# Kernel optimization log

Measured on AMD Instinct MI355X. Metric: run time of the kernel, lower is better.

## Reference

```python
import jax, jax.numpy as jnp
import numpy as np

N_NODES = 50000
SEQ_LEN = 20
INPUT_DIM = 16
HIDDEN = 128
LATENT = 64
N_EDGES = 800000


def setup_inputs() -> dict:
    key = jax.random.key(0)
    ks = iter(jax.random.split(key, 64))
    def p(shape, scale=0.05):
        return jax.random.normal(next(ks), shape, dtype=jnp.float32) * scale
    inp = {}
    inp['track_sequences'] = jax.random.normal(next(ks), (N_NODES, SEQ_LEN, INPUT_DIM), dtype=jnp.float32)
    inp['edge_index'] = jax.random.randint(next(ks), (2, N_EDGES), 0, N_NODES, dtype=jnp.int64)
    # LSTM (2 layers, torch gate order i,f,g,o)
    inp['lstm_Wih0'] = p((4 * HIDDEN, INPUT_DIM)); inp['lstm_Whh0'] = p((4 * HIDDEN, HIDDEN))
    inp['lstm_bih0'] = p((4 * HIDDEN,));            inp['lstm_bhh0'] = p((4 * HIDDEN,))
    inp['lstm_Wih1'] = p((4 * HIDDEN, HIDDEN));     inp['lstm_Whh1'] = p((4 * HIDDEN, HIDDEN))
    inp['lstm_bih1'] = p((4 * HIDDEN,));            inp['lstm_bhh1'] = p((4 * HIDDEN,))
    # encoder MLP: hidden->hidden->latent
    inp['enc_W1'] = p((HIDDEN, HIDDEN)); inp['enc_b1'] = p((HIDDEN,))
    inp['enc_W2'] = p((HIDDEN, LATENT)); inp['enc_b2'] = p((LATENT,))
    # 3 GCN layers
    inp['gcn_W0'] = p((LATENT, HIDDEN)); inp['gcn_b0'] = p((HIDDEN,))
    inp['gcn_W1'] = p((HIDDEN, HIDDEN)); inp['gcn_b1'] = p((HIDDEN,))
    inp['gcn_W2'] = p((HIDDEN, HIDDEN)); inp['gcn_b2'] = p((HIDDEN,))
    # edge predictor MLP: 2H -> H -> H/2 -> 1 (sigmoid)
    inp['e_W1'] = p((2 * HIDDEN, HIDDEN)); inp['e_b1'] = p((HIDDEN,))
    inp['e_W2'] = p((HIDDEN, HIDDEN // 2)); inp['e_b2'] = p((HIDDEN // 2,))
    inp['e_W3'] = p((HIDDEN // 2, 1)); inp['e_b3'] = p((1,))
    # classifier: H -> H/2 -> 4
    inp['c_W1'] = p((HIDDEN, HIDDEN // 2)); inp['c_b1'] = p((HIDDEN // 2,))
    inp['c_W2'] = p((HIDDEN // 2, 4)); inp['c_b2'] = p((4,))
    # uncertainty: H -> H/2 -> 1 (softplus)
    inp['u_W1'] = p((HIDDEN, HIDDEN // 2)); inp['u_b1'] = p((HIDDEN // 2,))
    inp['u_W2'] = p((HIDDEN // 2, 1)); inp['u_b2'] = p((1,))
    return inp


def _lstm_layer(x, Wih, Whh, bih, bhh):
    # x: [N, T, Din]; torch gate order i, f, g, o
    n, t, _ = x.shape
    h_dim = Whh.shape[1]
    xg = jnp.einsum('ntd,gd->ntg', x, Wih) + bih  # [N, T, 4H] precomputed input part
    def step(carry, xt):
        h, c = carry
        g = xt + h @ Whh.T + bhh
        i, f, gg, o = jnp.split(g, 4, axis=-1)
        c = jax.nn.sigmoid(f) * c + jax.nn.sigmoid(i) * jnp.tanh(gg)
        h = jax.nn.sigmoid(o) * jnp.tanh(c)
        return (h, c), h
    h0 = jnp.zeros((n, h_dim), x.dtype)
    (_, _), hs = jax.lax.scan(step, (h0, h0), jnp.swapaxes(xg, 0, 1))
    return jnp.swapaxes(hs, 0, 1)  # [N, T, H]


def _gcn(x, W, b, src, dst, num_nodes):
    # PyG GCNConv: self-loops, symmetric deg^-1/2 normalization
    x = x @ W  # [N, out]
    loop = jnp.arange(num_nodes, dtype=src.dtype)
    s = jnp.concatenate([src, loop])
    d = jnp.concatenate([dst, loop])
    deg = jax.ops.segment_sum(jnp.ones_like(d, x.dtype), d, num_segments=num_nodes)
    dinv = jax.lax.rsqrt(jnp.maximum(deg, 1.0))  # deg >= 1 due to self-loops
    norm = dinv[s] * dinv[d]  # [E+N]
    out = jax.ops.segment_sum(x[s] * norm[:, None], d, num_segments=num_nodes)
    return out + b


def reference(track_sequences, edge_index,
              lstm_Wih0, lstm_Whh0, lstm_bih0, lstm_bhh0,
              lstm_Wih1, lstm_Whh1, lstm_bih1, lstm_bhh1,
              enc_W1, enc_b1, enc_W2, enc_b2,
              gcn_W0, gcn_b0, gcn_W1, gcn_b1, gcn_W2, gcn_b2,
              e_W1, e_b1, e_W2, e_b2, e_W3, e_b3,
              c_W1, c_b1, c_W2, c_b2,
              u_W1, u_b1, u_W2, u_b2):
    n = track_sequences.shape[0]
    # --- TrackEncoder (eval mode: LSTM inter-layer dropout inactive) ---
    h = _lstm_layer(track_sequences, lstm_Wih0, lstm_Whh0, lstm_bih0, lstm_bhh0)
    h = _lstm_layer(h, lstm_Wih1, lstm_Whh1, lstm_bih1, lstm_bhh1)
    final_hidden = h[:, -1]  # [N, H]
    latent = jax.nn.relu(final_hidden @ enc_W1 + enc_b1) @ enc_W2 + enc_b2  # [N, L]
    # --- GCN stack (eval mode: dropout inactive) ---
    src, dst = edge_index[0], edge_index[1]
    x = latent
    for W, b in ((gcn_W0, gcn_b0), (gcn_W1, gcn_b1), (gcn_W2, gcn_b2)):
        x = jax.nn.relu(_gcn(x, W, b, src, dst, n))
    # --- edge predictor ---
    ef = jnp.concatenate([x[src], x[dst]], axis=1)  # [E, 2H]
    ef = jax.nn.relu(ef @ e_W1 + e_b1)
    ef = jax.nn.relu(ef @ e_W2 + e_b2)
    edge_pred = jax.nn.sigmoid(ef @ e_W3 + e_b3)  # [E, 1]
    # --- classifier & uncertainty heads ---
    track_classes = jax.nn.relu(x @ c_W1 + c_b1) @ c_W2 + c_b2  # [N, 4]
    uncertainties = jax.nn.softplus(jax.nn.relu(x @ u_W1 + u_b1) @ u_W2 + u_b2)  # [N, 1]
    return (x, edge_pred, track_classes, uncertainties)
```

## Files before the change

kernel.cpp:

```cpp
#include <hip/hip_runtime.h>
#include <math.h>

typedef float f32x4 __attribute__((ext_vector_type(4)));
typedef short s16x8 __attribute__((ext_vector_type(8)));
typedef unsigned short u16;

__device__ __forceinline__ float sigmoid_(float x) { return 1.f / (1.f + __expf(-x)); }
__device__ __forceinline__ float tanh_(float x) {
  float e = __expf(-2.f * x);
  return fmaf(2.f, 1.f / (1.f + e), -1.f);
}
__device__ __forceinline__ float softplus_(float x) {
  return (x > 15.f) ? x : log1pf(__expf(x));
}
__device__ __forceinline__ u16 f2bf(float f) {
  unsigned u = __float_as_uint(f);
  u += 0x7fffu + ((u >> 16) & 1u);
  return (u16)(u >> 16);
}
__device__ __forceinline__ float bf2f(u16 u) {
  return __uint_as_float((unsigned)u << 16);
}
#define PIN4(x) asm volatile("" : "+v"(x))

__global__ void prep_lstm_w(const float* __restrict__ Wih0, const float* __restrict__ Whh0,
                            const float* __restrict__ Wih1, const float* __restrict__ Whh1,
                            const float* __restrict__ bih0, const float* __restrict__ bhh0,
                            const float* __restrict__ bih1, const float* __restrict__ bhh1,
                            u16* __restrict__ Wp0, u16* __restrict__ Wp1,
                            float* __restrict__ bs0, float* __restrict__ bs1)
{
  int idx = blockIdx.x * 256 + threadIdx.x;
  if (idx < 20 * 512 * 8) {
    int c = idx >> 12, rem = idx & 4095;
    int col = rem >> 3, e = rem & 7;
    int k = c * 8 + e;
    float v = 0.f;
    if (k < 16) v = Wih0[col * 16 + k];
    else if (k >= 32) v = Whh0[col * 128 + (k - 32)];
    Wp0[idx] = f2bf(v);
  }
  int i1 = idx - 20 * 512 * 8;
  if (i1 >= 0 && i1 < 32 * 512 * 8) {
    int c = i1 >> 12, rem = i1 & 4095;
    int col = rem >> 3, e = rem & 7;
    int k = c * 8 + e;
    float v = (k < 128) ? Wih1[col * 128 + k] : Whh1[col * 128 + (k - 128)];
    Wp1[i1] = f2bf(v);
  }
  int i2 = idx - 52 * 512 * 8;
  if (i2 >= 0 && i2 < 512) bs0[i2] = bih0[i2] + bhh0[i2];
  int i3 = i2 - 512;
  if (i3 >= 0 && i3 < 512) bs1[i3] = bih1[i3] + bhh1[i3];
}

__global__ void pack_w(const float* __restrict__ W, u16* __restrict__ Wp, int K, int C) {
// ... 27 lines not shown
    cuW2p[j] = f2bf(v);
  }
  int j2 = idx - (128 * 128 + 2048);
  if (j2 >= 0 && j2 < 128) cub1[j2] = (j2 < 64) ? cb1[j2] : ub1[j2 - 64];
  int j3 = j2 - 128;
  if (j3 >= 0 && j3 < 16) cub2[j3] = (j3 < 4) ? cb2[j3] : (j3 == 4 ? ub2[0] : 0.f);
}

__device__ __forceinline__ void epi2(const f32x4 (&acc)[2][4], f32x4* cs,
    const float (&bs)[4], u16* ldsw, int uoff, int kq, int mh,
    int nodebase, float* hf, int u, int n, bool last)
{
#pragma unroll
  for (int mm = 0; mm < 2; ++mm) {
#pragma unroll
    for (int r = 0; r < 4; ++r) {
      float gi = acc[mm][0][r] + bs[0];
      float gf = acc[mm][1][r] + bs[1];
      float gg = acc[mm][2][r] + bs[2];
      float go = acc[mm][3][r] + bs[3];
      float c = sigmoid_(gf) * cs[mm][r] + sigmoid_(gi) * tanh_(gg);
      cs[mm][r] = c;
      float h = sigmoid_(go) * tanh_(c);
      int node = (mh * 2 + mm) * 16 + kq * 4 + r;
      ldsw[uoff + node * 8] = f2bf(h);
      if (last) {
        int gn = nodebase + node;
        if (gn < n) hf[(size_t)gn * 128 + u] = h;
      }
    }
  }
}

__global__ __launch_bounds__(512, 2) void lstm_l0(
    const float* __restrict__ seq, const u16* __restrict__ Wp0,
    const float* __restrict__ bs0, u16* __restrict__ h0seq,
    int n, int tile0, int ntiles)
{
  __shared__ __align__(16) u16 A0[2 * 20 * 512];
  const int RSZ = 20 * 512;
  const int tid = threadIdx.x;
  const int l = tid & 63;
  const int wq = __builtin_amdgcn_readfirstlane(tid >> 6);
  const int kq = l >> 4;
  const int la = (l & 15) * 8;
  const int colu = wq * 16 + (l & 15);
  const int uoff = (4 + (colu >> 3)) * 512 + (colu & 7);

  s16x8 b0[5][4];
#pragma unroll
  for (int kc = 0; kc < 5; ++kc)
#pragma unroll
    for (int g = 0; g < 4; ++g) {
      b0[kc][g] = *(const s16x8*)&Wp0[(size_t)(kc * 4 + kq) * 4096 + (g * 128 + colu) * 8];
      PIN4(b0[kc][g]);
    }
  float bsr[4];
#pragma unroll
  for (int g = 0; g < 4; ++g) bsr[g] = bs0[g * 128 + colu];
  const f32x4 zero4 = {0.f, 0.f, 0.f, 0.f};

  for (int tt = blockIdx.x; tt < ntiles; tt += gridDim.x) {
    const int nodebase = (tile0 + tt) * 64;
    const int nld = min(nodebase + (tid >> 2), n - 1);
    u16* __restrict__ hdst = h0seq + (size_t)tt * 20 * 8192;
    for (int i = tid; i < 18 * 512; i += 512) A0[2 * 512 + i] = 0;
    for (int i = tid; i < 2 * 512; i += 512) A0[RSZ + 2 * 512 + i] = 0;
    if (tid < 256) {
      int nd = tid >> 2, q = tid & 3;
      f32x4 v = __builtin_nontemporal_load((const f32x4*)(seq + (size_t)nld * 320 + q * 4));
      unsigned d0 = (unsigned)f2bf(v[0]) | ((unsigned)f2bf(v[1]) << 16);
      unsigned d1 = (unsigned)f2bf(v[2]) | ((unsigned)f2bf(v[3]) << 16);
      unsigned* dstp = (unsigned*)&A0[(q >> 1) * 512 + nd * 8 + (q & 1) * 4];
      dstp[0] = d0; dstp[1] = d1;
    }
    f32x4 c0[4];
#pragma unroll
    for (int m = 0; m < 4; ++m) c0[m] = zero4;
    __syncthreads();

    for (int t = 0; t < 20; ++t) {
      const int base_r = (t & 1) * RSZ;
      const int base_w = ((t + 1) & 1) * RSZ;
      f32x4 xnext;
      const bool ldx = (t < 19) && (tid < 256);
      if (ldx) xnext = __builtin_nontemporal_load(
          (const f32x4*)(seq + (size_t)nld * 320 + (t + 1) * 16 + (tid & 3) * 4));
      if (t >= 1) {
        s16x8 u0 = *(const s16x8*)&A0[base_r + 2048 + tid * 8];
        s16x8 u1 = *(const s16x8*)&A0[base_r + 2048 + 4096 + tid * 8];
        __builtin_nontemporal_store(u0, (s16x8*)&hdst[(size_t)(t - 1) * 8192 + tid * 8]);
        __builtin_nontemporal_store(u1, (s16x8*)&hdst[(size_t)(t - 1) * 8192 + 4096 + tid * 8]);
      }
#pragma unroll
      for (int mh = 0; mh < 2; ++mh) {
        f32x4 acc[2][4];
#pragma unroll
        for (int mm = 0; mm < 2; ++mm)
#pragma unroll
          for (int g = 0; g < 4; ++g) acc[mm][g] = zero4;
#pragma unroll
        for (int kc = 0; kc < 5; ++kc) {
          const int ch = kc * 4 + kq;
          s16x8 av[2];
#pragma unroll
          for (int mm = 0; mm < 2; ++mm)
            av[mm] = *(const s16x8*)&A0[base_r + ch * 512 + (mh * 2 + mm) * 128 + la];
#pragma unroll
          for (int g = 0; g < 4; ++g)
#pragma unroll
            for (int mm = 0; mm < 2; ++mm)
              acc[mm][g] = __builtin_amdgcn_mfma_f32_16x16x32_bf16(av[mm], b0[kc][g], acc[mm][g], 0, 0, 0);
        }
        epi2(acc, &c0[mh * 2], bsr, &A0[base_w], uoff, kq, mh, 0, nullptr, colu, 0, false);
      }
      if (ldx) {
        int nd = tid >> 2, q = tid & 3;
        unsigned d0 = (unsigned)f2bf(xnext[0]) | ((unsigned)f2bf(xnext[1]) << 16);
        unsigned d1 = (unsigned)f2bf(xnext[2]) | ((unsigned)f2bf(xnext[3]) << 16);
        unsigned* dstp = (unsigned*)&A0[base_w + (q >> 1) * 512 + nd * 8 + (q & 1) * 4];
        dstp[0] = d0; dstp[1] = d1;
      }
      __syncthreads();
    }
    {
      s16x8 u0 = *(const s16x8*)&A0[2048 + tid * 8];
      s16x8 u1 = *(const s16x8*)&A0[2048 + 4096 + tid * 8];
      __builtin_nontemporal_store(u0, (s16x8*)&hdst[(size_t)19 * 8192 + tid * 8]);
      __builtin_nontemporal_store(u1, (s16x8*)&hdst[(size_t)19 * 8192 + 4096 + tid * 8]);
    }
    __syncthreads();
  }
}

__global__ __launch_bounds__(512, 2) void lstm_l1(
    const u16* __restrict__ h0seq, const u16* __restrict__ Wp1,
    const float* __restrict__ bs1, float* __restrict__ hfinal,
    int n, int tile0, int ntiles)
{
  __shared__ __align__(16) u16 A1[2 * 32 * 512];
  const int RSZ = 32 * 512;
  const int tid = threadIdx.x;
  const int l = tid & 63;
  const int wq = __builtin_amdgcn_readfirstlane(tid >> 6);
  const int kq = l >> 4;
  const int la = (l & 15) * 8;
  const int colu = wq * 16 + (l & 15);
  const int uoff = (16 + (colu >> 3)) * 512 + (colu & 7);

  s16x8 b1[8][4];
#pragma unroll
  for (int kc = 0; kc < 8; ++kc)
#pragma unroll
    for (int g = 0; g < 4; ++g) {
      b1[kc][g] = *(const s16x8*)&Wp1[(size_t)(kc * 4 + kq) * 4096 + (g * 128 + colu) * 8];
      PIN4(b1[kc][g]);
    }
  float bsr[4];
#pragma unroll
  for (int g = 0; g < 4; ++g) bsr[g] = bs1[g * 128 + colu];
  const f32x4 zero4 = {0.f, 0.f, 0.f, 0.f};

  for (int tt = blockIdx.x; tt < ntiles; tt += gridDim.x) {
    const int nodebase = (tile0 + tt) * 64;
    const u16* __restrict__ hsrc = h0seq + (size_t)tt * 20 * 8192;
    for (int i = tid; i < 16 * 512; i += 512) A1[16 * 512 + i] = 0;
    {
      s16x8 s0 = __builtin_nontemporal_load((const s16x8*)&hsrc[tid * 8]);
      s16x8 s1 = __builtin_nontemporal_load((const s16x8*)&hsrc[4096 + tid * 8]);
      *(s16x8*)&A1[tid * 8] = s0;
      *(s16x8*)&A1[4096 + tid * 8] = s1;
    }
    f32x4 c1[4];
#pragma unroll
    for (int m = 0; m < 4; ++m) c1[m] = zero4;
    __syncthreads();

    for (int t = 0; t < 20; ++t) {
      const int base_r = (t & 1) * RSZ;
      const int base_w = ((t + 1) & 1) * RSZ;
      s16x8 p0, p1;
      const bool ld = (t < 19);
      if (ld) {
        p0 = __builtin_nontemporal_load((const s16x8*)&hsrc[(size_t)(t + 1) * 8192 + tid * 8]);
        p1 = __builtin_nontemporal_load((const s16x8*)&hsrc[(size_t)(t + 1) * 8192 + 4096 + tid * 8]);
      }
#pragma unroll
      for (int mh = 0; mh < 2; ++mh) {
        f32x4 acc[2][4];
#pragma unroll
        for (int mm = 0; mm < 2; ++mm)
#pragma unroll
          for (int g = 0; g < 4; ++g) acc[mm][g] = zero4;
#pragma unroll
        for (int kc = 0; kc < 8; ++kc) {
          const int ch = kc * 4 + kq;
          s16x8 av[2];
#pragma unroll
          for (int mm = 0; mm < 2; ++mm)
            av[mm] = *(const s16x8*)&A1[base_r + ch * 512 + (mh * 2 + mm) * 128 + la];
#pragma unroll
          for (int g = 0; g < 4; ++g)
#pragma unroll
            for (int mm = 0; mm < 2; ++mm)
              acc[mm][g] = __builtin_amdgcn_mfma_f32_16x16x32_bf16(av[mm], b1[kc][g], acc[mm][g], 0, 0, 0);
        }
        epi2(acc, &c1[mh * 2], bsr, &A1[base_w], uoff, kq, mh, nodebase, hfinal, colu, n, t == 19);
      }
      if (ld) {
        *(s16x8*)&A1[base_w + tid * 8] = p0;
        *(s16x8*)&A1[base_w + 4096 + tid * 8] = p1;
      }
      __syncthreads();
    }
  }
}

template<int KD, int COLS, bool INBF, bool OUTBF, bool RELU, bool BIAS>
__global__ __launch_bounds__(COLS * 4, 4) void ngemm_m(
    const void* __restrict__ xin_, const u16* __restrict__ Wp,
    const float* __restrict__ b, void* __restrict__ out_, int n)
{
  constexpr int NT = COLS * 4;
  __shared__ __align__(16) u16 A[(KD / 8) * 512];
  const int tid = threadIdx.x;
  const int l = tid & 63;
  const int wq = __builtin_amdgcn_readfirstlane(tid >> 6);
  const int kq = l >> 4;
  const int la = (l & 15) * 8;
  const int colu = wq * 16 + (l & 15);
  const int nodebase = blockIdx.x * 64;

  for (int s = tid; s < 64 * KD / 8; s += NT) {
    int nd = s / (KD / 8), q = s % (KD / 8);
    int gn = min(nodebase + nd, n - 1);
    if (INBF) {
      const u16* xp = (const u16*)xin_ + (size_t)gn * KD + q * 8;
      *(s16x8*)&A[q * 512 + nd * 8] = *(const s16x8*)xp;
    } else {
      const float* xp = (const float*)xin_ + (size_t)gn * KD + q * 8;
      float4 v0 = *(const float4*)xp;
      float4 v1 = *(const float4*)(xp + 4);
      s16x8 pk;
      pk[0] = (short)f2bf(v0.x); pk[1] = (short)f2bf(v0.y);
// ... 17 lines not shown
    for (int m = 0; m < 4; ++m) {
      s16x8 av = *(const s16x8*)&A[ch * 512 + m * 128 + la];
      acc[m] = __builtin_amdgcn_mfma_f32_16x16x32_bf16(av, bv, acc[m], 0, 0, 0);
    }
  }
  float bb = BIAS ? b[colu] : 0.f;
#pragma unroll
  for (int m = 0; m < 4; ++m)
#pragma unroll
    for (int r = 0; r < 4; ++r) {
      int gn = nodebase + m * 16 + kq * 4 + r;
      if (gn < n) {
        float v = acc[m][r] + bb;
        if (RELU) v = fmaxf(v, 0.f);
        if (OUTBF) ((u16*)out_)[(size_t)gn * COLS + colu] = f2bf(v);
        else       ((float*)out_)[(size_t)gn * COLS + colu] = v;
      }
    }
}

__global__ void deg_count(const int* __restrict__ dst, float* __restrict__ deg, int ne, int n) {
  int i = blockIdx.x * 256 + threadIdx.x;
  if (i < ne) {
    int d = dst[i]; d = min(max(d, 0), n - 1);
    atomicAdd(deg + d, 1.f);
  }
}

__global__ void dinv_k(const float* __restrict__ deg, float* __restrict__ dinv, int n) {
  int i = blockIdx.x * 256 + threadIdx.x;
  if (i < n) dinv[i] = rsqrtf(deg[i] + 1.f);
}

__global__ void scan_k(const float* __restrict__ deg, int* __restrict__ rowptr, int n) {
  __shared__ int sh[1024];
  __shared__ int carry;
  const int tid = threadIdx.x;
  if (tid == 0) carry = 0;
  __syncthreads();
  for (int base = 0; base < n; base += 1024) {
    int i = base + tid;
    int v = (i < n) ? (int)deg[i] : 0;
    sh[tid] = v;
    __syncthreads();
    for (int off = 1; off < 1024; off <<= 1) {
      int t = (tid >= off) ? sh[tid - off] : 0;
      __syncthreads();
      sh[tid] += t;
      __syncthreads();
    }
    if (i < n) rowptr[i] = carry + sh[tid] - v;
    int tot = sh[1023];
    __syncthreads();
    if (tid == 0) carry += tot;
    __syncthreads();
  }
  if (tid == 0) rowptr[n] = carry;
}

__global__ void fill_k(const int* __restrict__ src, const int* __restrict__ dst,
                       const int* __restrict__ rowptr, int* __restrict__ cursor,
                       const float* __restrict__ dinv,
                       int* __restrict__ cidx, float* __restrict__ enrm, int ne, int n) {
  int i = blockIdx.x * 256 + threadIdx.x;
  if (i < ne) {
    int s = min(max(src[i], 0), n - 1);
    int d = min(max(dst[i], 0), n - 1);
    int p = atomicAdd(cursor + d, 1);
    int o = rowptr[d] + p;
    cidx[o] = s;
    enrm[o] = dinv[s] * dinv[d];
  }
}

template<bool OUT32>
__global__ __launch_bounds__(256, 4) void gcn_gather_bf(
    const u16* __restrict__ y, const int* __restrict__ rowptr,
    const int* __restrict__ cidx, const float* __restrict__ enrm,
    const float* __restrict__ dinv, const float* __restrict__ b,
    void* __restrict__ out, int n)
{
  const int l = threadIdx.x & 63;
  const int wq = threadIdx.x >> 6;
  const int node = blockIdx.x * 4 + wq;
  if (node >= n) return;
  float dv = dinv[node];
  unsigned su = ((const unsigned*)(y + (size_t)node * 128))[l];
  float ax = bf2f((u16)(su & 0xffff)) * dv * dv;
  float ay = bf2f((u16)(su >> 16)) * dv * dv;
  int r0 = rowptr[node], r1 = rowptr[node + 1];
// ... 237 lines not shown
  const float* eb2   = (const float*)d_in[23];
  const float* eW3   = (const float*)d_in[24];
  const float* eb3   = (const float*)d_in[25];
  const float* cW1   = (const float*)d_in[26];
  const float* cb1   = (const float*)d_in[27];
  const float* cW2   = (const float*)d_in[28];
  const float* cb2   = (const float*)d_in[29];
  const float* uW1   = (const float*)d_in[30];
  const float* ub1   = (const float*)d_in[31];
  const float* uW2   = (const float*)d_in[32];
  const float* ub2   = (const float*)d_in[33];

  const int n  = in_sizes[0] / 320;
  const int ne = in_sizes[1] / 2;
  const int* src = eidx;
  const int* dst = eidx + ne;

  char* ws = (char*)d_ws;
  size_t off = 0;
  auto alloc = [&](size_t elems) -> float* {
    float* p = (float*)(ws + off);
    off += ((elems * 4 + 255) & ~(size_t)255);
    return p;
  };
  const size_t nb = (size_t)n * 128;
  float* B1     = alloc(nb);
  float* B2     = alloc(nb);
  float* B4     = alloc(nb);
  float* latent = alloc((size_t)n * 64);
  float* deg    = alloc(n);
  float* dinv   = alloc(n);
  int*   rowptr = (int*)alloc(n + 1);
  int*   cursor = (int*)alloc(n);
  int*   cidx   = (int*)alloc(ne);
  float* enrm   = alloc(ne);
  u16* Wp0    = (u16*)alloc(20 * 512 * 8 / 2);
  u16* Wp1    = (u16*)alloc(32 * 512 * 8 / 2);
  u16* encW1p = (u16*)alloc(128 * 128 / 2);
  u16* encW2p = (u16*)alloc(128 * 64 / 2);
  u16* gW0p   = (u16*)alloc(64 * 128 / 2);
  u16* gW1p   = (u16*)alloc(128 * 128 / 2);
  u16* gW2p   = (u16*)alloc(128 * 128 / 2);
  u16* eW1tp  = (u16*)alloc(128 * 128 / 2);
  u16* eW1bp  = (u16*)alloc(128 * 128 / 2);
  u16* eW2p   = (u16*)alloc(128 * 64 / 2);
  u16* cuW1p  = (u16*)alloc(128 * 128 / 2);
  u16* cuW2p  = (u16*)alloc(1024);
  float* cub1  = alloc(128);
  float* cub2  = alloc(16);
  float* bsum0 = alloc(512);
  float* bsum1 = alloc(512);
  (void)n_in; (void)out_size;

  float* xout = (float*)d_out;
  float* ep   = xout + nb;
  float* cls  = ep + ne;
  float* unc  = cls + (size_t)n * 4;

  auto PK = [&](const float* s, u16* d, int K, int C) {
    pack_w<<<dim3((K * C + 255) / 256), dim3(256), 0, stream>>>(s, d, K, C);
  };
  PK(encW1, encW1p, 128, 128);
  PK(encW2, encW2p, 128, 64);
  PK(gW0,   gW0p,   64, 128);
  PK(gW1,   gW1p,   128, 128);
  PK(gW2,   gW2p,   128, 128);
  PK(eW1,             eW1tp, 128, 128);
  PK(eW1 + 128 * 128, eW1bp, 128, 128);
  PK(eW2,   eW2p,   128, 64);
  pack_headw<<<dim3((128 * 128 + 2048 + 128 + 16 + 255) / 256), dim3(256), 0, stream>>>(
      cW1, cb1, cW2, cb2, uW1, ub1, uW2, ub2, cuW1p, cub1, cuW2p, cub2);

  prep_lstm_w<<<dim3((52 * 512 * 8 + 1024 + 255) / 256), dim3(256), 0, stream>>>(
      Wih0, Whh0, Wih1, Whh1, bih0, bhh0, bih1, bhh1, Wp0, Wp1, bsum0, bsum1);

  hipMemsetAsync(deg, 0, (size_t)n * 4, stream);
  deg_count<<<dim3((ne + 255) / 256), dim3(256), 0, stream>>>(dst, deg, ne, n);
  dinv_k<<<dim3((n + 255) / 256), dim3(256), 0, stream>>>(deg, dinv, n);
  scan_k<<<dim3(1), dim3(1024), 0, stream>>>(deg, rowptr, n);
  hipMemsetAsync(cursor, 0, (size_t)n * 4, stream);
  fill_k<<<dim3((ne + 255) / 256), dim3(256), 0, stream>>>(
      src, dst, rowptr, cursor, dinv, cidx, enrm, ne, n);

  const int nblk = (n + 63) / 64;
  const int ntiles = nblk;

  const size_t per_tile = (size_t)20 * 8192 * sizeof(u16);
  size_t avail = (ws_size > off) ? (ws_size - off) : 0;
  int slab_tiles = (int)((avail / per_tile < (size_t)ntiles) ? (avail / per_tile) : (size_t)ntiles);
  if (slab_tiles < 1) slab_tiles = 1;
  {
    u16* h0seq = (u16*)(ws + off);
    for (int t0 = 0; t0 < ntiles; t0 += slab_tiles) {
      int st = (ntiles - t0 < slab_tiles) ? (ntiles - t0) : slab_tiles;
      int grid = (st < 512) ? st : 512;
      lstm_l0<<<dim3(grid), dim3(512), 0, stream>>>(seq, Wp0, bsum0, h0seq, n, t0, st);
      lstm_l1<<<dim3(grid), dim3(512), 0, stream>>>(h0seq, Wp1, bsum1, B1, n, t0, st);
    }
  }

  u16* t1b = (u16*)B2;
  u16* xb  = (u16*)B1;
  u16* yb  = (u16*)B2;
  u16* xb2 = (u16*)B4;
  u16* Pb  = (u16*)B1;
  u16* Qb  = (u16*)B4;
  ngemm_m<128, 128, false, true, true, true><<<dim3(nblk), dim3(512), 0, stream>>>(B1, encW1p, encb1, t1b, n);
  ngemm_m<128, 64, true, false, false, true><<<dim3(nblk), dim3(256), 0, stream>>>(t1b, encW2p, encb2, latent, n);

  const int gblk = (n + 3) / 4;
  gather64_k<<<dim3(gblk), dim3(256), 0, stream>>>(latent, rowptr, cidx, enrm, dinv, B2, n);
  ngemm_m<64, 128, false, true, true, true><<<dim3(nblk), dim3(512), 0, stream>>>(B2, gW0p, gb0, xb, n);
  ngemm_m<128, 128, true, true, false, false><<<dim3(nblk), dim3(512), 0, stream>>>(xb, gW1p, nullptr, yb, n);
  gcn_gather_bf<false><<<dim3(gblk), dim3(256), 0, stream>>>(yb, rowptr, cidx, enrm, dinv, gb1, xb2, n);
  ngemm_m<128, 128, true, true, false, false><<<dim3(nblk), dim3(512), 0, stream>>>(xb2, gW2p, nullptr, yb, n);
  gcn_gather_bf<true><<<dim3(gblk), dim3(256), 0, stream>>>(yb, rowptr, cidx, enrm, dinv, gb2, xout, n);

  ngemm_m<128, 128, false, true, false, false><<<dim3(nblk), dim3(512), 0, stream>>>(xout, eW1tp, nullptr, Pb, n);
  ngemm_m<128, 128, false, true, false, false><<<dim3(nblk), dim3(512), 0, stream>>>(xout, eW1bp, nullptr, Qb, n);
  edge_head_m<<<dim3((ne + 63) / 64), dim3(256), 0, stream>>>(
      Pb, Qb, src, dst, eb1, eW2p, eb2, eW3, eb3, ep, ne, n);

  node_heads_m<<<dim3(nblk), dim3(512), 0, stream>>>(
      xout, cuW1p, cub1, cuW2p, cub2, cls, unc, n);
}
```

Before: 2.029 ms.

## Fuse both LSTM layers into one wavefront-specialized pipelined kernel

Replaces the separate layer-0 and layer-1 LSTM kernels with one 1024-thread kernel. Waves 0-7 compute layer 0 and waves 8-15 compute layer 1, with layer 1 running one timestep behind and reading layer-0 hidden states directly from LDS. This removes the global round trip of the full layer-0 hidden sequence and the slab loop. In exchange, the weights are no longer pinned in registers and are reloaded from global/L2 at every step, and occupancy drops to one block per CU.

```diff
diff --git a/kernel.cpp b/kernel.cpp
--- a/kernel.cpp
+++ b/kernel.cpp
@@ -21,7 +21,6 @@
 __device__ __forceinline__ float bf2f(u16 u) {
   return __uint_as_float((unsigned)u << 16);
 }
-#define PIN4(x) asm volatile("" : "+v"(x))
 
 __global__ void prep_lstm_w(const float* __restrict__ Wih0, const float* __restrict__ Whh0,
                             const float* __restrict__ Wih1, const float* __restrict__ Whh1,
@@ -115,184 +114,117 @@
   }
 }
 
-__global__ __launch_bounds__(512, 2) void lstm_l0(
+__global__ __launch_bounds__(1024, 1) void lstm_fused2(
     const float* __restrict__ seq, const u16* __restrict__ Wp0,
-    const float* __restrict__ bs0, u16* __restrict__ h0seq,
-    int n, int tile0, int ntiles)
-{
-  __shared__ __align__(16) u16 A0[2 * 20 * 512];
-  const int RSZ = 20 * 512;
+    const u16* __restrict__ Wp1, const float* __restrict__ bs0,
+    const float* __restrict__ bs1, float* __restrict__ hfinal,
+    int n, int ntiles)
+{
+  __shared__ __align__(16) u16 R0[2][20 * 512];
+  __shared__ __align__(16) u16 R1[2][16 * 512];
   const int tid = threadIdx.x;
   const int l = tid & 63;
   const int wq = __builtin_amdgcn_readfirstlane(tid >> 6);
+  const int layer = wq >> 3;
+  const int lw = wq & 7;
   const int kq = l >> 4;
   const int la = (l & 15) * 8;
-  const int colu = wq * 16 + (l & 15);
-  const int uoff = (4 + (colu >> 3)) * 512 + (colu & 7);
-
-  s16x8 b0[5][4];
-#pragma unroll
-  for (int kc = 0; kc < 5; ++kc)
-#pragma unroll
-    for (int g = 0; g < 4; ++g) {
-      b0[kc][g] = *(const s16x8*)&Wp0[(size_t)(kc * 4 + kq) * 4096 + (g * 128 + colu) * 8];
-      PIN4(b0[kc][g]);
-    }
+  const int colu = lw * 16 + (l & 15);
+  const int uoff = layer ? ((colu >> 3) * 512 + (colu & 7))
+                         : ((4 + (colu >> 3)) * 512 + (colu & 7));
+  const u16* __restrict__ Wb = layer ? Wp1 : Wp0;
   float bsr[4];
 #pragma unroll
-  for (int g = 0; g < 4; ++g) bsr[g] = bs0[g * 128 + colu];
+  for (int g = 0; g < 4; ++g) bsr[g] = (layer ? bs1 : bs0)[g * 128 + colu];
   const f32x4 zero4 = {0.f, 0.f, 0.f, 0.f};
 
-  for (int tt = blockIdx.x; tt < ntiles; tt += gridDim.x) {
-    const int nodebase = (tile0 + tt) * 64;
+  for (int tile = blockIdx.x; tile < ntiles; tile += gridDim.x) {
+    const int nodebase = tile * 64;
     const int nld = min(nodebase + (tid >> 2), n - 1);
-    u16* __restrict__ hdst = h0seq + (size_t)tt * 20 * 8192;
-    for (int i = tid; i < 18 * 512; i += 512) A0[2 * 512 + i] = 0;
-    for (int i = tid; i < 2 * 512; i += 512) A0[RSZ + 2 * 512 + i] = 0;
+    for (int i = tid; i < 18 * 512; i += 1024) R0[0][2 * 512 + i] = 0;
+    for (int i = tid; i < 2 * 512; i += 1024) R0[1][2 * 512 + i] = 0;
+    for (int i = tid; i < 16 * 512; i += 1024) R1[0][i] = 0;
     if (tid < 256) {
       int nd = tid >> 2, q = tid & 3;
       f32x4 v = __builtin_nontemporal_load((const f32x4*)(seq + (size_t)nld * 320 + q * 4));
       unsigned d0 = (unsigned)f2bf(v[0]) | ((unsigned)f2bf(v[1]) << 16);
       unsigned d1 = (unsigned)f2bf(v[2]) | ((unsigned)f2bf(v[3]) << 16);
-      unsigned* dstp = (unsigned*)&A0[(q >> 1) * 512 + nd * 8 + (q & 1) * 4];
+      unsigned* dstp = (unsigned*)&R0[0][(q >> 1) * 512 + nd * 8 + (q & 1) * 4];
       dstp[0] = d0; dstp[1] = d1;
     }
-    f32x4 c0[4];
-#pragma unroll
-    for (int m = 0; m < 4; ++m) c0[m] = zero4;
+    f32x4 cst[4];
+#pragma unroll
+    for (int m = 0; m < 4; ++m) cst[m] = zero4;
     __syncthreads();
 
-    for (int t = 0; t < 20; ++t) {
-      const int base_r = (t & 1) * RSZ;
-      const int base_w = ((t + 1) & 1) * RSZ;
-      f32x4 xnext;
-      const bool ldx = (t < 19) && (tid < 256);
-      if (ldx) xnext = __builtin_nontemporal_load(
-          (const f32x4*)(seq + (size_t)nld * 320 + (t + 1) * 16 + (tid & 3) * 4));
-      if (t >= 1) {
-        s16x8 u0 = *(const s16x8*)&A0[base_r + 2048 + tid * 8];
-        s16x8 u1 = *(const s16x8*)&A0[base_r + 2048 + 4096 + tid * 8];
-        __builtin_nontemporal_store(u0, (s16x8*)&hdst[(size_t)(t - 1) * 8192 + tid * 8]);
-        __builtin_nontemporal_store(u1, (s16x8*)&hdst[(size_t)(t - 1) * 8192 + 4096 + tid * 8]);
-      }
-#pragma unroll
-      for (int mh = 0; mh < 2; ++mh) {
-        f32x4 acc[2][4];
-#pragma unroll
-        for (int mm = 0; mm < 2; ++mm)
-#pragma unroll
-          for (int g = 0; g < 4; ++g) acc[mm][g] = zero4;
-#pragma unroll
-        for (int kc = 0; kc < 5; ++kc) {
-          const int ch = kc * 4 + kq;
-          s16x8 av[2];
-#pragma unroll
-          for (int mm = 0; mm < 2; ++mm)
-            av[mm] = *(const s16x8*)&A0[base_r + ch * 512 + (mh * 2 + mm) * 128 + la];
-#pragma unroll
-          for (int g = 0; g < 4; ++g)
+    for (int s = 0; s < 21; ++s) {
+      const int r = s & 1, w = r ^ 1;
+      if (layer == 0) {
+        if (s < 20) {
+          f32x4 xn;
+          const bool ldx = (s < 19) && (tid < 256);
+          if (ldx) xn = __builtin_nontemporal_load(
+              (const f32x4*)(seq + (size_t)nld * 320 + (s + 1) * 16 + (tid & 3) * 4));
+#pragma unroll
+          for (int mh = 0; mh < 2; ++mh) {
+            f32x4 acc[2][4];
 #pragma unroll
             for (int mm = 0; mm < 2; ++mm)
-              acc[mm][g] = __builtin_amdgcn_mfma_f32_16x16x32_bf16(av[mm], b0[kc][g], acc[mm][g], 0, 0, 0);
+#pragma unroll
+              for (int g = 0; g < 4; ++g) acc[mm][g] = zero4;
+#pragma unroll
+            for (int kc = 0; kc < 5; ++kc) {
+              const int ch = kc * 4 + kq;
+              s16x8 av[2];
+#pragma unroll
+              for (int mm = 0; mm < 2; ++mm)
+                av[mm] = *(const s16x8*)&R0[r][ch * 512 + (mh * 2 + mm) * 128 + la];
+#pragma unroll
+              for (int g = 0; g < 4; ++g) {
+                s16x8 bv = *(const s16x8*)&Wb[(size_t)ch * 4096 + (g * 128 + colu) * 8];
+#pragma unroll
+                for (int mm = 0; mm < 2; ++mm)
+                  acc[mm][g] = __builtin_amdgcn_mfma_f32_16x16x32_bf16(av[mm], bv, acc[mm][g], 0, 0, 0);
+              }
+            }
+            epi2(acc, &cst[mh * 2], bsr, &R0[w][0], uoff, kq, mh, 0, nullptr, colu, 0, false);
+          }
+          if (ldx) {
+            int nd = tid >> 2, q = tid & 3;
+            unsigned d0 = (unsigned)f2bf(xn[0]) | ((unsigned)f2bf(xn[1]) << 16);
+            unsigned d1 = (unsigned)f2bf(xn[2]) | ((unsigned)f2bf(xn[3]) << 16);
+            unsigned* dstp = (unsigned*)&R0[w][(q >> 1) * 512 + nd * 8 + (q & 1) * 4];
+            dstp[0] = d0; dstp[1] = d1;
+          }
         }
-        epi2(acc, &c0[mh * 2], bsr, &A0[base_w], uoff, kq, mh, 0, nullptr, colu, 0, false);
-      }
-      if (ldx) {
-        int nd = tid >> 2, q = tid & 3;
-        unsigned d0 = (unsigned)f2bf(xnext[0]) | ((unsigned)f2bf(xnext[1]) << 16);
-        unsigned d1 = (unsigned)f2bf(xnext[2]) | ((unsigned)f2bf(xnext[3]) << 16);
-        unsigned* dstp = (unsigned*)&A0[base_w + (q >> 1) * 512 + nd * 8 + (q & 1) * 4];
-        dstp[0] = d0; dstp[1] = d1;
-      }
-      __syncthreads();
-    }
-    {
-      s16x8 u0 = *(const s16x8*)&A0[2048 + tid * 8];
-      s16x8 u1 = *(const s16x8*)&A0[2048 + 4096 + tid * 8];
-      __builtin_nontemporal_store(u0, (s16x8*)&hdst[(size_t)19 * 8192 + tid * 8]);
-      __builtin_nontemporal_store(u1, (s16x8*)&hdst[(size_t)19 * 8192 + 4096 + tid * 8]);
-    }
-    __syncthreads();
-  }
-}
-
-__global__ __launch_bounds__(512, 2) void lstm_l1(
-    const u16* __restrict__ h0seq, const u16* __restrict__ Wp1,
-    const float* __restrict__ bs1, float* __restrict__ hfinal,
-    int n, int tile0, int ntiles)
-{
-  __shared__ __align__(16) u16 A1[2 * 32 * 512];
-  const int RSZ = 32 * 512;
-  const int tid = threadIdx.x;
-  const int l = tid & 63;
-  const int wq = __builtin_amdgcn_readfirstlane(tid >> 6);
-  const int kq = l >> 4;
-  const int la = (l & 15) * 8;
-  const int colu = wq * 16 + (l & 15);
-  const int uoff = (16 + (colu >> 3)) * 512 + (colu & 7);
-
-  s16x8 b1[8][4];
-#pragma unroll
-  for (int kc = 0; kc < 8; ++kc)
-#pragma unroll
-    for (int g = 0; g < 4; ++g) {
-      b1[kc][g] = *(const s16x8*)&Wp1[(size_t)(kc * 4 + kq) * 4096 + (g * 128 + colu) * 8];
-      PIN4(b1[kc][g]);
-    }
-  float bsr[4];
-#pragma unroll
-  for (int g = 0; g < 4; ++g) bsr[g] = bs1[g * 128 + colu];
-  const f32x4 zero4 = {0.f, 0.f, 0.f, 0.f};
-
-  for (int tt = blockIdx.x; tt < ntiles; tt += gridDim.x) {
-    const int nodebase = (tile0 + tt) * 64;
-    const u16* __restrict__ hsrc = h0seq + (size_t)tt * 20 * 8192;
-    for (int i = tid; i < 16 * 512; i += 512) A1[16 * 512 + i] = 0;
-    {
-      s16x8 s0 = __builtin_nontemporal_load((const s16x8*)&hsrc[tid * 8]);
-      s16x8 s1 = __builtin_nontemporal_load((const s16x8*)&hsrc[4096 + tid * 8]);
-      *(s16x8*)&A1[tid * 8] = s0;
-      *(s16x8*)&A1[4096 + tid * 8] = s1;
-    }
-    f32x4 c1[4];
-#pragma unroll
-    for (int m = 0; m < 4; ++m) c1[m] = zero4;
-    __syncthreads();
-
-    for (int t = 0; t < 20; ++t) {
-      const int base_r = (t & 1) * RSZ;
-      const int base_w = ((t + 1) & 1) * RSZ;
-      s16x8 p0, p1;
-      const bool ld = (t < 19);
-      if (ld) {
-        p0 = __builtin_nontemporal_load((const s16x8*)&hsrc[(size_t)(t + 1) * 8192 + tid * 8]);
-        p1 = __builtin_nontemporal_load((const s16x8*)&hsrc[(size_t)(t + 1) * 8192 + 4096 + tid * 8]);
-      }
-#pragma unroll
-      for (int mh = 0; mh < 2; ++mh) {
-        f32x4 acc[2][4];
-#pragma unroll
-        for (int mm = 0; mm < 2; ++mm)
-#pragma unroll
-          for (int g = 0; g < 4; ++g) acc[mm][g] = zero4;
-#pragma unroll
-        for (int kc = 0; kc < 8; ++kc) {
-          const int ch = kc * 4 + kq;
-          s16x8 av[2];
-#pragma unroll
-          for (int mm = 0; mm < 2; ++mm)
-            av[mm] = *(const s16x8*)&A1[base_r + ch * 512 + (mh * 2 + mm) * 128 + la];
-#pragma unroll
-          for (int g = 0; g < 4; ++g)
+      } else {
+        if (s >= 1) {
+#pragma unroll
+          for (int mh = 0; mh < 2; ++mh) {
+            f32x4 acc[2][4];
 #pragma unroll
             for (int mm = 0; mm < 2; ++mm)
-              acc[mm][g] = __builtin_amdgcn_mfma_f32_16x16x32_bf16(av[mm], b1[kc][g], acc[mm][g], 0, 0, 0);
+#pragma unroll
+              for (int g = 0; g < 4; ++g) acc[mm][g] = zero4;
+#pragma unroll
+            for (int kc = 0; kc < 8; ++kc) {
+              const int ch = kc * 4 + kq;
+              const u16* Ab = (kc < 4) ? &R0[r][(4 + ch) * 512] : &R1[w][(ch - 16) * 512];
+              s16x8 av[2];
+#pragma unroll
+              for (int mm = 0; mm < 2; ++mm)
+                av[mm] = *(const s16x8*)&Ab[(mh * 2 + mm) * 128 + la];
+#pragma unroll
+              for (int g = 0; g < 4; ++g) {
+                s16x8 bv = *(const s16x8*)&Wb[(size_t)ch * 4096 + (g * 128 + colu) * 8];
+#pragma unroll
+                for (int mm = 0; mm < 2; ++mm)
+                  acc[mm][g] = __builtin_amdgcn_mfma_f32_16x16x32_bf16(av[mm], bv, acc[mm][g], 0, 0, 0);
+              }
+            }
+            epi2(acc, &cst[mh * 2], bsr, &R1[r][0], uoff, kq, mh, nodebase, hfinal, colu, n, s == 20);
+          }
         }
-        epi2(acc, &c1[mh * 2], bsr, &A1[base_w], uoff, kq, mh, nodebase, hfinal, colu, n, t == 19);
-      }
-      if (ld) {
-        *(s16x8*)&A1[base_w + tid * 8] = p0;
-        *(s16x8*)&A1[base_w + 4096 + tid * 8] = p1;
       }
       __syncthreads();
     }
@@ -721,7 +653,7 @@
   float* cub2  = alloc(16);
   float* bsum0 = alloc(512);
   float* bsum1 = alloc(512);
-  (void)n_in; (void)out_size;
+  (void)n_in; (void)out_size; (void)ws_size;
 
   float* xout = (float*)d_out;
   float* ep   = xout + nb;
@@ -756,18 +688,10 @@
   const int nblk = (n + 63) / 64;
   const int ntiles = nblk;
 
-  const size_t per_tile = (size_t)20 * 8192 * sizeof(u16);
-  size_t avail = (ws_size > off) ? (ws_size - off) : 0;
-  int slab_tiles = (int)((avail / per_tile < (size_t)ntiles) ? (avail / per_tile) : (size_t)ntiles);
-  if (slab_tiles < 1) slab_tiles = 1;
   {
-    u16* h0seq = (u16*)(ws + off);
-    for (int t0 = 0; t0 < ntiles; t0 += slab_tiles) {
-      int st = (ntiles - t0 < slab_tiles) ? (ntiles - t0) : slab_tiles;
-      int grid = (st < 512) ? st : 512;
-      lstm_l0<<<dim3(grid), dim3(512), 0, stream>>>(seq, Wp0, bsum0, h0seq, n, t0, st);
-      lstm_l1<<<dim3(grid), dim3(512), 0, stream>>>(h0seq, Wp1, bsum1, B1, n, t0, st);
-    }
+    int grid = (ntiles < 2048) ? ntiles : 2048;
+    lstm_fused2<<<dim3(grid), dim3(1024), 0, stream>>>(
+        seq, Wp0, Wp1, bsum0, bsum1, B1, n, ntiles);
   }
 
   u16* t1b = (u16*)B2;
```

New measurement: 2.924 ms. 1.44x slower.

## Halve LSTM block size, stream weights from global, parallelize degree scan

Applied to the files above, without the earlier changes.

The two LSTM kernels now run 4 waves of 256 threads instead of 8. Each wave covers 32 hidden units in two column groups. The recurrent weight fragments are no longer held pinned in registers; they are reloaded from global memory (through cache) inside every k-chunk of every timestep. This lowers register pressure, but each block does twice the MFMA work per step with half the waves, and weight traffic rises. Separately, the single-block serial prefix scan over node degrees is replaced with a three-kernel scan (partial sums, exclusive scan of those sums, final per-block scan) to remove a serial bottleneck.

```diff
diff --git a/kernel.cpp b/kernel.cpp
--- a/kernel.cpp
+++ b/kernel.cpp
@@ -21,7 +21,6 @@
 __device__ __forceinline__ float bf2f(u16 u) {
   return __uint_as_float((unsigned)u << 16);
 }
-#define PIN4(x) asm volatile("" : "+v"(x))
 
 __global__ void prep_lstm_w(const float* __restrict__ Wih0, const float* __restrict__ Whh0,
                             const float* __restrict__ Wih1, const float* __restrict__ Whh1,
@@ -115,7 +114,7 @@
   }
 }
 
-__global__ __launch_bounds__(512, 2) void lstm_l0(
+__global__ __launch_bounds__(256, 2) void lstm_l0(
     const float* __restrict__ seq, const u16* __restrict__ Wp0,
     const float* __restrict__ bs0, u16* __restrict__ h0seq,
     int n, int tile0, int ntiles)
@@ -124,32 +123,24 @@
   const int RSZ = 20 * 512;
   const int tid = threadIdx.x;
   const int l = tid & 63;
-  const int wq = __builtin_amdgcn_readfirstlane(tid >> 6);
+  const int wv = __builtin_amdgcn_readfirstlane(tid >> 6);
   const int kq = l >> 4;
   const int la = (l & 15) * 8;
-  const int colu = wq * 16 + (l & 15);
-  const int uoff = (4 + (colu >> 3)) * 512 + (colu & 7);
-
-  s16x8 b0[5][4];
-#pragma unroll
-  for (int kc = 0; kc < 5; ++kc)
-#pragma unroll
-    for (int g = 0; g < 4; ++g) {
-      b0[kc][g] = *(const s16x8*)&Wp0[(size_t)(kc * 4 + kq) * 4096 + (g * 128 + colu) * 8];
-      PIN4(b0[kc][g]);
-    }
-  float bsr[4];
-#pragma unroll
-  for (int g = 0; g < 4; ++g) bsr[g] = bs0[g * 128 + colu];
+  float bsr[2][4];
+#pragma unroll
+  for (int cg = 0; cg < 2; ++cg)
+#pragma unroll
+    for (int g = 0; g < 4; ++g)
+      bsr[cg][g] = bs0[g * 128 + wv * 32 + cg * 16 + (l & 15)];
   const f32x4 zero4 = {0.f, 0.f, 0.f, 0.f};
 
   for (int tt = blockIdx.x; tt < ntiles; tt += gridDim.x) {
     const int nodebase = (tile0 + tt) * 64;
     const int nld = min(nodebase + (tid >> 2), n - 1);
     u16* __restrict__ hdst = h0seq + (size_t)tt * 20 * 8192;
-    for (int i = tid; i < 18 * 512; i += 512) A0[2 * 512 + i] = 0;
-    for (int i = tid; i < 2 * 512; i += 512) A0[RSZ + 2 * 512 + i] = 0;
-    if (tid < 256) {
+    for (int i = tid; i < 18 * 512; i += 256) A0[2 * 512 + i] = 0;
+    for (int i = tid; i < 2 * 512; i += 256) A0[RSZ + 2 * 512 + i] = 0;
+    {
       int nd = tid >> 2, q = tid & 3;
       f32x4 v = __builtin_nontemporal_load((const f32x4*)(seq + (size_t)nld * 320 + q * 4));
       unsigned d0 = (unsigned)f2bf(v[0]) | ((unsigned)f2bf(v[1]) << 16);
@@ -157,45 +148,56 @@
       unsigned* dstp = (unsigned*)&A0[(q >> 1) * 512 + nd * 8 + (q & 1) * 4];
       dstp[0] = d0; dstp[1] = d1;
     }
-    f32x4 c0[4];
-#pragma unroll
-    for (int m = 0; m < 4; ++m) c0[m] = zero4;
+    f32x4 c0[2][4];
+#pragma unroll
+    for (int cg = 0; cg < 2; ++cg)
+#pragma unroll
+      for (int m = 0; m < 4; ++m) c0[cg][m] = zero4;
     __syncthreads();
 
     for (int t = 0; t < 20; ++t) {
       const int base_r = (t & 1) * RSZ;
       const int base_w = ((t + 1) & 1) * RSZ;
       f32x4 xnext;
-      const bool ldx = (t < 19) && (tid < 256);
+      const bool ldx = (t < 19);
       if (ldx) xnext = __builtin_nontemporal_load(
           (const f32x4*)(seq + (size_t)nld * 320 + (t + 1) * 16 + (tid & 3) * 4));
       if (t >= 1) {
-        s16x8 u0 = *(const s16x8*)&A0[base_r + 2048 + tid * 8];
-        s16x8 u1 = *(const s16x8*)&A0[base_r + 2048 + 4096 + tid * 8];
-        __builtin_nontemporal_store(u0, (s16x8*)&hdst[(size_t)(t - 1) * 8192 + tid * 8]);
-        __builtin_nontemporal_store(u1, (s16x8*)&hdst[(size_t)(t - 1) * 8192 + 4096 + tid * 8]);
-      }
-#pragma unroll
-      for (int mh = 0; mh < 2; ++mh) {
-        f32x4 acc[2][4];
-#pragma unroll
-        for (int mm = 0; mm < 2; ++mm)
-#pragma unroll
-          for (int g = 0; g < 4; ++g) acc[mm][g] = zero4;
-#pragma unroll
-        for (int kc = 0; kc < 5; ++kc) {
-          const int ch = kc * 4 + kq;
-          s16x8 av[2];
+#pragma unroll
+        for (int k = 0; k < 4; ++k) {
+          int j = tid + k * 256;
+          s16x8 u0 = *(const s16x8*)&A0[base_r + 2048 + j * 8];
+          __builtin_nontemporal_store(u0, (s16x8*)&hdst[(size_t)(t - 1) * 8192 + j * 8]);
+        }
+      }
+#pragma unroll
+      for (int cg = 0; cg < 2; ++cg) {
+        const int colu = wv * 32 + cg * 16 + (l & 15);
+        const int uoff = (4 + (colu >> 3)) * 512 + (colu & 7);
+#pragma unroll
+        for (int mh = 0; mh < 2; ++mh) {
+          f32x4 acc[2][4];
 #pragma unroll
           for (int mm = 0; mm < 2; ++mm)
-            av[mm] = *(const s16x8*)&A0[base_r + ch * 512 + (mh * 2 + mm) * 128 + la];
-#pragma unroll
-          for (int g = 0; g < 4; ++g)
+#pragma unroll
+            for (int g = 0; g < 4; ++g) acc[mm][g] = zero4;
+#pragma unroll
+          for (int kc = 0; kc < 5; ++kc) {
+            const int ch = kc * 4 + kq;
+            s16x8 av[2];
 #pragma unroll
             for (int mm = 0; mm < 2; ++mm)
-              acc[mm][g] = __builtin_amdgcn_mfma_f32_16x16x32_bf16(av[mm], b0[kc][g], acc[mm][g], 0, 0, 0);
+              av[mm] = *(const s16x8*)&A0[base_r + ch * 512 + (mh * 2 + mm) * 128 + la];
+#pragma unroll
+            for (int g = 0; g < 4; ++g) {
+              s16x8 bv = *(const s16x8*)&Wp0[(size_t)ch * 4096 + (g * 128 + colu) * 8];
+#pragma unroll
+              for (int mm = 0; mm < 2; ++mm)
+                acc[mm][g] = __builtin_amdgcn_mfma_f32_16x16x32_bf16(av[mm], bv, acc[mm][g], 0, 0, 0);
+            }
+          }
+          epi2(acc, &c0[cg][mh * 2], bsr[cg], &A0[base_w], uoff, kq, mh, 0, nullptr, colu, 0, false);
         }
-        epi2(acc, &c0[mh * 2], bsr, &A0[base_w], uoff, kq, mh, 0, nullptr, colu, 0, false);
       }
       if (ldx) {
         int nd = tid >> 2, q = tid & 3;
@@ -207,16 +209,18 @@
       __syncthreads();
     }
     {
-      s16x8 u0 = *(const s16x8*)&A0[2048 + tid * 8];
-      s16x8 u1 = *(const s16x8*)&A0[2048 + 4096 + tid * 8];
-      __builtin_nontemporal_store(u0, (s16x8*)&hdst[(size_t)19 * 8192 + tid * 8]);
-      __builtin_nontemporal_store(u1, (s16x8*)&hdst[(size_t)19 * 8192 + 4096 + tid * 8]);
+#pragma unroll
+      for (int k = 0; k < 4; ++k) {
+        int j = tid + k * 256;
+        s16x8 u0 = *(const s16x8*)&A0[2048 + j * 8];
+        __builtin_nontemporal_store(u0, (s16x8*)&hdst[(size_t)19 * 8192 + j * 8]);
+      }
     }
     __syncthreads();
   }
 }
 
-__global__ __launch_bounds__(512, 2) void lstm_l1(
+__global__ __launch_bounds__(256, 2) void lstm_l1(
     const u16* __restrict__ h0seq, const u16* __restrict__ Wp1,
     const float* __restrict__ bs1, float* __restrict__ hfinal,
     int n, int tile0, int ntiles)
@@ -225,74 +229,79 @@
   const int RSZ = 32 * 512;
   const int tid = threadIdx.x;
   const int l = tid & 63;
-  const int wq = __builtin_amdgcn_readfirstlane(tid >> 6);
+  const int wv = __builtin_amdgcn_readfirstlane(tid >> 6);
   const int kq = l >> 4;
   const int la = (l & 15) * 8;
-  const int colu = wq * 16 + (l & 15);
-  const int uoff = (16 + (colu >> 3)) * 512 + (colu & 7);
-
-  s16x8 b1[8][4];
-#pragma unroll
-  for (int kc = 0; kc < 8; ++kc)
-#pragma unroll
-    for (int g = 0; g < 4; ++g) {
-      b1[kc][g] = *(const s16x8*)&Wp1[(size_t)(kc * 4 + kq) * 4096 + (g * 128 + colu) * 8];
-      PIN4(b1[kc][g]);
-    }
-  float bsr[4];
-#pragma unroll
-  for (int g = 0; g < 4; ++g) bsr[g] = bs1[g * 128 + colu];
+  float bsr[2][4];
+#pragma unroll
+  for (int cg = 0; cg < 2; ++cg)
+#pragma unroll
+    for (int g = 0; g < 4; ++g)
+      bsr[cg][g] = bs1[g * 128 + wv * 32 + cg * 16 + (l & 15)];
   const f32x4 zero4 = {0.f, 0.f, 0.f, 0.f};
 
   for (int tt = blockIdx.x; tt < ntiles; tt += gridDim.x) {
     const int nodebase = (tile0 + tt) * 64;
     const u16* __restrict__ hsrc = h0seq + (size_t)tt * 20 * 8192;
-    for (int i = tid; i < 16 * 512; i += 512) A1[16 * 512 + i] = 0;
-    {
-      s16x8 s0 = __builtin_nontemporal_load((const s16x8*)&hsrc[tid * 8]);
-      s16x8 s1 = __builtin_nontemporal_load((const s16x8*)&hsrc[4096 + tid * 8]);
-      *(s16x8*)&A1[tid * 8] = s0;
-      *(s16x8*)&A1[4096 + tid * 8] = s1;
-    }
-    f32x4 c1[4];
-#pragma unroll
-    for (int m = 0; m < 4; ++m) c1[m] = zero4;
+    for (int i = tid; i < 16 * 512; i += 256) A1[16 * 512 + i] = 0;
+#pragma unroll
+    for (int k = 0; k < 4; ++k) {
+      int j = tid + k * 256;
+      s16x8 s0 = __builtin_nontemporal_load((const s16x8*)&hsrc[j * 8]);
+      *(s16x8*)&A1[j * 8] = s0;
+    }
+    f32x4 c1[2][4];
+#pragma unroll
+    for (int cg = 0; cg < 2; ++cg)
+#pragma unroll
+      for (int m = 0; m < 4; ++m) c1[cg][m] = zero4;
     __syncthreads();
 
     for (int t = 0; t < 20; ++t) {
       const int base_r = (t & 1) * RSZ;
       const int base_w = ((t + 1) & 1) * RSZ;
-      s16x8 p0, p1;
+      s16x8 p[4];
       const bool ld = (t < 19);
       if (ld) {
-        p0 = __builtin_nontemporal_load((const s16x8*)&hsrc[(size_t)(t + 1) * 8192 + tid * 8]);
-        p1 = __builtin_nontemporal_load((const s16x8*)&hsrc[(size_t)(t + 1) * 8192 + 4096 + tid * 8]);
-      }
-#pragma unroll
-      for (int mh = 0; mh < 2; ++mh) {
-        f32x4 acc[2][4];
-#pragma unroll
-        for (int mm = 0; mm < 2; ++mm)
-#pragma unroll
-          for (int g = 0; g < 4; ++g) acc[mm][g] = zero4;
-#pragma unroll
-        for (int kc = 0; kc < 8; ++kc) {
-          const int ch = kc * 4 + kq;
-          s16x8 av[2];
+#pragma unroll
+        for (int k = 0; k < 4; ++k)
+          p[k] = __builtin_nontemporal_load(
+              (const s16x8*)&hsrc[(size_t)(t + 1) * 8192 + (tid + k * 256) * 8]);
+      }
+#pragma unroll
+      for (int cg = 0; cg < 2; ++cg) {
+        const int colu = wv * 32 + cg * 16 + (l & 15);
+        const int uoff = (16 + (colu >> 3)) * 512 + (colu & 7);
+#pragma unroll
+        for (int mh = 0; mh < 2; ++mh) {
+          f32x4 acc[2][4];
 #pragma unroll
           for (int mm = 0; mm < 2; ++mm)
-            av[mm] = *(const s16x8*)&A1[base_r + ch * 512 + (mh * 2 + mm) * 128 + la];
-#pragma unroll
-          for (int g = 0; g < 4; ++g)
+#pragma unroll
+            for (int g = 0; g < 4; ++g) acc[mm][g] = zero4;
+#pragma unroll
+          for (int kc = 0; kc < 8; ++kc) {
+            const int ch = kc * 4 + kq;
+            s16x8 av[2];
 #pragma unroll
             for (int mm = 0; mm < 2; ++mm)
-              acc[mm][g] = __builtin_amdgcn_mfma_f32_16x16x32_bf16(av[mm], b1[kc][g], acc[mm][g], 0, 0, 0);
+              av[mm] = *(const s16x8*)&A1[base_r + ch * 512 + (mh * 2 + mm) * 128 + la];
+#pragma unroll
+            for (int g = 0; g < 4; ++g) {
+              s16x8 bv = *(const s16x8*)&Wp1[(size_t)ch * 4096 + (g * 128 + colu) * 8];
+#pragma unroll
+              for (int mm = 0; mm < 2; ++mm)
+                acc[mm][g] = __builtin_amdgcn_mfma_f32_16x16x32_bf16(av[mm], bv, acc[mm][g], 0, 0, 0);
+            }
+          }
+          epi2(acc, &c1[cg][mh * 2], bsr[cg], &A1[base_w], uoff, kq, mh,
+               nodebase, hfinal, colu, n, t == 19);
         }
-        epi2(acc, &c1[mh * 2], bsr, &A1[base_w], uoff, kq, mh, nodebase, hfinal, colu, n, t == 19);
       }
       if (ld) {
-        *(s16x8*)&A1[base_w + tid * 8] = p0;
-        *(s16x8*)&A1[base_w + 4096 + tid * 8] = p1;
+#pragma unroll
+        for (int k = 0; k < 4; ++k)
+          *(s16x8*)&A1[base_w + (tid + k * 256) * 8] = p[k];
       }
       __syncthreads();
     }
@@ -376,30 +385,55 @@
   if (i < n) dinv[i] = rsqrtf(deg[i] + 1.f);
 }
 
-__global__ void scan_k(const float* __restrict__ deg, int* __restrict__ rowptr, int n) {
+__global__ void scan_part(const float* __restrict__ deg, int* __restrict__ part, int n) {
+  __shared__ int sh[256];
+  const int tid = threadIdx.x;
+  const int base = blockIdx.x * 1024;
+  int s = 0;
+  for (int j = tid; j < 1024; j += 256) {
+    int i = base + j;
+    s += (i < n) ? (int)deg[i] : 0;
+  }
+  sh[tid] = s;
+  __syncthreads();
+  for (int off = 128; off > 0; off >>= 1) {
+    if (tid < off) sh[tid] += sh[tid + off];
+    __syncthreads();
+  }
+  if (tid == 0) part[blockIdx.x] = sh[0];
+}
+
+__global__ void scan_exc(int* __restrict__ part, int nb, int* __restrict__ rowptr, int n) {
+  __shared__ int sh[256];
+  const int tid = threadIdx.x;
+  int v = (tid < nb) ? part[tid] : 0;
+  sh[tid] = v;
+  __syncthreads();
+  for (int off = 1; off < 256; off <<= 1) {
+    int t = (tid >= off) ? sh[tid - off] : 0;
+    __syncthreads();
+    sh[tid] += t;
+    __syncthreads();
+  }
+  if (tid < nb) part[tid] = sh[tid] - v;
+  if (tid == 255) rowptr[n] = sh[255];
+}
+
+__global__ void scan_final(const float* __restrict__ deg, const int* __restrict__ part,
+                           int* __restrict__ rowptr, int n) {
   __shared__ int sh[1024];
-  __shared__ int carry;
   const int tid = threadIdx.x;
-  if (tid == 0) carry = 0;
+  const int i = blockIdx.x * 1024 + tid;
+  int v = (i < n) ? (int)deg[i] : 0;
+  sh[tid] = v;
   __syncthreads();
-  for (int base = 0; base < n; base += 1024) {
-    int i = base + tid;
-    int v = (i < n) ? (int)deg[i] : 0;
-    sh[tid] = v;
+  for (int off = 1; off < 1024; off <<= 1) {
+    int t = (tid >= off) ? sh[tid - off] : 0;
     __syncthreads();
-    for (int off = 1; off < 1024; off <<= 1) {
-      int t = (tid >= off) ? sh[tid - off] : 0;
-      __syncthreads();
-      sh[tid] += t;
-      __syncthreads();
-    }
-    if (i < n) rowptr[i] = carry + sh[tid] - v;
-    int tot = sh[1023];
+    sh[tid] += t;
     __syncthreads();
-    if (tid == 0) carry += tot;
-    __syncthreads();
-  }
-  if (tid == 0) rowptr[n] = carry;
+  }
+  if (i < n) rowptr[i] = part[blockIdx.x] + sh[tid] - v;
 }
 
 __global__ void fill_k(const int* __restrict__ src, const int* __restrict__ dst,
@@ -703,6 +737,7 @@
   float* dinv   = alloc(n);
   int*   rowptr = (int*)alloc(n + 1);
   int*   cursor = (int*)alloc(n);
+  int*   part   = (int*)alloc(256);
   int*   cidx   = (int*)alloc(ne);
   float* enrm   = alloc(ne);
   u16* Wp0    = (u16*)alloc(20 * 512 * 8 / 2);
@@ -748,7 +783,10 @@
   hipMemsetAsync(deg, 0, (size_t)n * 4, stream);
   deg_count<<<dim3((ne + 255) / 256), dim3(256), 0, stream>>>(dst, deg, ne, n);
   dinv_k<<<dim3((n + 255) / 256), dim3(256), 0, stream>>>(deg, dinv, n);
-  scan_k<<<dim3(1), dim3(1024), 0, stream>>>(deg, rowptr, n);
+  const int nsb = (n + 1023) / 1024;
+  scan_part<<<dim3(nsb), dim3(256), 0, stream>>>(deg, part, n);
+  scan_exc<<<dim3(1), dim3(256), 0, stream>>>(part, nsb, rowptr, n);
+  scan_final<<<dim3(nsb), dim3(1024), 0, stream>>>(deg, part, rowptr, n);
   hipMemsetAsync(cursor, 0, (size_t)n * 4, stream);
   fill_k<<<dim3((ne + 255) / 256), dim3(256), 0, stream>>>(
       src, dst, rowptr, cursor, dinv, cidx, enrm, ne, n);
@@ -765,8 +803,8 @@
     for (int t0 = 0; t0 < ntiles; t0 += slab_tiles) {
       int st = (ntiles - t0 < slab_tiles) ? (ntiles - t0) : slab_tiles;
       int grid = (st < 512) ? st : 512;
-      lstm_l0<<<dim3(grid), dim3(512), 0, stream>>>(seq, Wp0, bsum0, h0seq, n, t0, st);
-      lstm_l1<<<dim3(grid), dim3(512), 0, stream>>>(h0seq, Wp1, bsum1, B1, n, t0, st);
+      lstm_l0<<<dim3(grid), dim3(256), 0, stream>>>(seq, Wp0, bsum0, h0seq, n, t0, st);
+      lstm_l1<<<dim3(grid), dim3(256), 0, stream>>>(h0seq, Wp1, bsum1, B1, n, t0, st);
     }
   }
 
```

Result: slower. 3.332 ms (+64.2%).
